# Performance work log

Measured on AMD Instinct MI355X. Metric: run time of the kernel, lower is better.

## Reference

```python
import jax, jax.numpy as jnp
import numpy as np

REG1 = 0.05
REG2 = 0.05

N, D, P = 262144, 256, 512


def setup_inputs() -> dict:
    key = jax.random.key(0)
    kz, kp = jax.random.split(key)
    z = jax.random.normal(kz, (N, D), dtype=jnp.float32)
    # nn.Parameter(torch.rand(P, D)) -> uniform [0, 1)
    prototype_vectors = jax.random.uniform(kp, (P, D), dtype=jnp.float32)
    return {"z": z, "prototype_vectors": prototype_vectors}


def _cdist(a, b):
    # Euclidean pairwise distances [Na, Nb] via the norm trick (matches torch.cdist p=2).
    a2 = jnp.sum(a * a, axis=-1, keepdims=True)          # [Na, 1]
    b2 = jnp.sum(b * b, axis=-1)[None, :]                # [1, Nb]
    sq = a2 + b2 - 2.0 * (a @ b.T)
    return jnp.sqrt(jnp.maximum(sq, 0.0))


def reference(z, prototype_vectors):
    p_dist = _cdist(z, prototype_vectors)                # [N, P]
    f_dist = _cdist(prototype_vectors, z)                # [P, N]
    return (REG1 * jnp.mean(jnp.min(p_dist, axis=1))
            + REG2 * jnp.mean(jnp.min(f_dist, axis=1)))
```

## Files before the change

### kernel.cpp

```cpp
#include <hip/hip_runtime.h>
#include <hip/hip_bf16.h>

#define N_ROWS 262144
#define DDIM   256
#define PROTO  512
#define BM     64
#define RTG    4096
#define NBLK   8192

typedef __bf16 bf16x8 __attribute__((ext_vector_type(8)));
typedef float  f32x4  __attribute__((ext_vector_type(4)));

__global__ void prep_proto(const float* __restrict__ Pm,
                           unsigned short* __restrict__ PBf,
                           float* __restrict__ P2) {
  int p = blockIdx.x;
  int k = threadIdx.x;
  float v = Pm[p * DDIM + k];
  int idx = (p >> 4) * 4096 + (k >> 5) * 512 + ((((k >> 3) & 3) * 16) + (p & 15)) * 8 + (k & 7);
  ((__bf16*)PBf)[idx] = (__bf16)v;
  float sq = v * v;
  #pragma unroll
  for (int m = 1; m < 64; m <<= 1) sq += __shfl_xor(sq, m);
  __shared__ float ws4[4];
  if ((k & 63) == 0) ws4[k >> 6] = sq;
  __syncthreads();
  if (k == 0) P2[p] = (ws4[0] + ws4[1]) + (ws4[2] + ws4[3]);
}

__global__ __launch_bounds__(256, 4)
void proto_main(const float* __restrict__ Z, const unsigned short* __restrict__ PBf,
                const float* __restrict__ P2, float* __restrict__ colpart,
                float* __restrict__ rowminpart) {
  __shared__ __align__(16) unsigned short A_lds[BM * 256];
  __shared__ float z2s[BM];
  __shared__ float rowred[BM * 4];

  const int t   = threadIdx.x;
  const int w   = t >> 6;
  const int l   = t & 63;
  const int l15 = l & 15;
  const int lg  = l >> 4;

  const int bid = blockIdx.x;
  const int g   = ((bid >> 4) << 3) | (bid & 7);
  const int cc  = (bid >> 3) & 1;
  const size_t row0 = (size_t)g * BM;

  const int srow = t >> 2;
  const int sc4  = t & 3;
  {
    const float4* Zv = (const float4*)Z + (row0 + srow) * (DDIM / 4);
    float4 za[16];
    #pragma unroll
    for (int m = 0; m < 8; ++m) {
      za[2 * m]     = Zv[(sc4 + m * 4) * 2];
      za[2 * m + 1] = Zv[(sc4 + m * 4) * 2 + 1];
    }
    float zacc = 0.f;
    #pragma unroll
    for (int m = 0; m < 8; ++m) {
      float4 a0 = za[2 * m], a1 = za[2 * m + 1];
      zacc += a0.x*a0.x + a0.y*a0.y + a0.z*a0.z + a0.w*a0.w
            + a1.x*a1.x + a1.y*a1.y + a1.z*a1.z + a1.w*a1.w;
      bf16x8 pk;
      pk[0] = (__bf16)a0.x; pk[1] = (__bf16)a0.y; pk[2] = (__bf16)a0.z; pk[3] = (__bf16)a0.w;
      pk[4] = (__bf16)a1.x; pk[5] = (__bf16)a1.y; pk[6] = (__bf16)a1.z; pk[7] = (__bf16)a1.w;
      int slot = (sc4 + m * 4) ^ (srow & 7);
      *(bf16x8*)&A_lds[srow * 256 + slot * 8] = pk;
    }
    zacc += __shfl_xor(zacc, 1);
    zacc += __shfl_xor(zacc, 2);
    if (sc4 == 0) z2s[srow] = zacc;
  }

  float p2r[4];
  #pragma unroll
  for (int j = 0; j < 4; ++j) p2r[j] = P2[cc * 256 + w * 64 + j * 16 + l15];

  __syncthreads();

  f32x4 acc[4][4];
  #pragma unroll
  for (int i = 0; i < 4; ++i)
    #pragma unroll
    for (int j = 0; j < 4; ++j)
      acc[i][j] = (f32x4){0.f, 0.f, 0.f, 0.f};

  const unsigned short* PBw = PBf + (size_t)(cc * 16 + w * 4) * 4096 + l * 8;
  bf16x8 bgn[4];
  #pragma unroll
  for (int j = 0; j < 4; ++j)
    bgn[j] = *(const bf16x8*)&PBw[(size_t)(j * 8) * 512];
  #pragma unroll
  for (int ks = 0; ks < 8; ++ks) {
    bf16x8 bgc[4];
    #pragma unroll
    for (int j = 0; j < 4; ++j) bgc[j] = bgn[j];
    if (ks < 7) {
      #pragma unroll
      for (int j = 0; j < 4; ++j)
        bgn[j] = *(const bf16x8*)&PBw[(size_t)(j * 8 + ks + 1) * 512];
    }
    __builtin_amdgcn_s_setprio(1);
    #pragma unroll
    for (int i = 0; i < 4; ++i) {
      bf16x8 af = *(const bf16x8*)&A_lds[(i * 16 + l15) * 256 + (((ks * 4 + lg) ^ (l15 & 7)) * 8)];
      #pragma unroll
      for (int j = 0; j < 4; ++j)
        acc[i][j] = __builtin_amdgcn_mfma_f32_16x16x32_bf16(af, bgc[j], acc[i][j], 0, 0, 0);
    }
    __builtin_amdgcn_s_setprio(0);
  }

  float cmin[4] = {3.4e38f, 3.4e38f, 3.4e38f, 3.4e38f};
  #pragma unroll
  for (int i = 0; i < 4; ++i) {
    #pragma unroll
    for (int r = 0; r < 4; ++r) {
      int arow = i * 16 + lg * 4 + r;
      float z2 = z2s[arow];
      float m = 3.4e38f;
      #pragma unroll
      for (int j = 0; j < 4; ++j) {
        float sq = fmaxf(z2 + p2r[j] - 2.0f * acc[i][j][r], 0.0f);
        m = fminf(m, sq);
        cmin[j] = fminf(cmin[j], sq);
      }
      m = fminf(m, __shfl_xor(m, 1));
      m = fminf(m, __shfl_xor(m, 2));
      m = fminf(m, __shfl_xor(m, 4));
      m = fminf(m, __shfl_xor(m, 8));
      if (l15 == 0) rowred[arow * 4 + w] = m;
    }
  }
  #pragma unroll
  for (int j = 0; j < 4; ++j) {
    float c = cmin[j];
    c = fminf(c, __shfl_xor(c, 16));
    c = fminf(c, __shfl_xor(c, 32));
    cmin[j] = c;
  }
  if (l < 16) {
    #pragma unroll
    for (int j = 0; j < 4; ++j)
      colpart[(size_t)g * PROTO + cc * 256 + w * 64 + j * 16 + l] = cmin[j];
  }
  __syncthreads();
  if (t < 64) {
    float m = fminf(fminf(rowred[t * 4], rowred[t * 4 + 1]),
                    fminf(rowred[t * 4 + 2], rowred[t * 4 + 3]));
    rowminpart[(size_t)cc * N_ROWS + row0 + t] = m;
  }
}

__global__ void col_reduce(const float* __restrict__ colpart, float* __restrict__ colfin) {
  int t    = threadIdx.x;
  int colb = blockIdx.x * 16;
  int cl   = t & 15;
  int gg   = t >> 4;
  float m = 3.4e38f;
  for (int g = gg; g < RTG; g += 32)
    m = fminf(m, colpart[(size_t)g * PROTO + colb + cl]);
  m = fminf(m, __shfl_xor(m, 16));
  m = fminf(m, __shfl_xor(m, 32));
  __shared__ float red[8][16];
  if ((t & 63) < 16) red[t >> 6][cl] = m;
  __syncthreads();
  if (t < 16) {
    float r = red[0][t];
    #pragma unroll
    for (int wv = 1; wv < 8; ++wv) r = fminf(r, red[wv][t]);
    colfin[colb + t] = sqrtf(r);
  }
}

__global__ void row_reduce(const float* __restrict__ rowminpart, float* __restrict__ rowsum) {
  int t = threadIdx.x;
  size_t grow = (size_t)blockIdx.x * 256 + t;
  float m = fminf(rowminpart[grow], rowminpart[N_ROWS + grow]);
  float s = sqrtf(m);
  #pragma unroll
  for (int mm = 1; mm < 64; mm <<= 1) s += __shfl_xor(s, mm);
  __shared__ float ws4[4];
  if ((t & 63) == 0) ws4[t >> 6] = s;
  __syncthreads();
  if (t == 0) rowsum[blockIdx.x] = (ws4[0] + ws4[1]) + (ws4[2] + ws4[3]);
}

__global__ void final_reduce(const float* __restrict__ colfin,
                             const float* __restrict__ rowsum,
                             float* __restrict__ out) {
  int t = threadIdx.x;
  float sc = colfin[t];
  float sr = rowsum[t] + rowsum[t + 512];
  #pragma unroll
  for (int mm = 1; mm < 64; mm <<= 1) { sc += __shfl_xor(sc, mm); sr += __shfl_xor(sr, mm); }
  __shared__ float wc[8], wr[8];
  if ((t & 63) == 0) { wc[t >> 6] = sc; wr[t >> 6] = sr; }
  __syncthreads();
  if (t == 0) {
    float tc = 0.f, tr = 0.f;
    #pragma unroll
    for (int i = 0; i < 8; ++i) { tc += wc[i]; tr += wr[i]; }
    out[0] = 0.05f * (tr / (float)N_ROWS) + 0.05f * (tc / (float)PROTO);
  }
}

extern "C" void kernel_launch(void* const* d_in, const int* in_sizes, int n_in,
                              void* d_out, int out_size, void* d_ws, size_t ws_size,
                              hipStream_t stream) {
  const float* z  = (const float*)d_in[0];
  const float* pv = (const float*)d_in[1];
  char* ws = (char*)d_ws;
  size_t off = 0;
  unsigned short* PBf = (unsigned short*)(ws + off); off += 262144;
  float* P2           = (float*)(ws + off);          off += 2048;
  float* colpart      = (float*)(ws + off);          off += (size_t)RTG * PROTO * 4;
  float* colfin       = (float*)(ws + off);          off += 2048;
  float* rowminpart   = (float*)(ws + off);          off += (size_t)2 * N_ROWS * 4;
  float* rowsum       = (float*)(ws + off);          off += 4096;

  prep_proto<<<PROTO, DDIM, 0, stream>>>(pv, PBf, P2);
  proto_main<<<NBLK, 256, 0, stream>>>(z, PBf, P2, colpart, rowminpart);
  col_reduce<<<32, 512, 0, stream>>>(colpart, colfin);
  row_reduce<<<N_ROWS / 256, 256, 0, stream>>>(rowminpart, rowsum);
  final_reduce<<<1, PROTO, 0, stream>>>(colfin, rowsum, (float*)d_out);
}
```

Before: 140.6 us.

## Double row tile per block to 128 rows with eight waves

```diff
diff --git a/kernel.cpp b/kernel.cpp
--- a/kernel.cpp
+++ b/kernel.cpp
@@ -4,9 +4,9 @@
 #define N_ROWS 262144
 #define DDIM   256
 #define PROTO  512
-#define BM     64
-#define RTG    4096
-#define NBLK   8192
+#define BM2    128
+#define RTG    2048
+#define NBLK   4096
 
 typedef __bf16 bf16x8 __attribute__((ext_vector_type(8)));
 typedef float  f32x4  __attribute__((ext_vector_type(4)));
@@ -28,24 +28,27 @@
   if (k == 0) P2[p] = (ws4[0] + ws4[1]) + (ws4[2] + ws4[3]);
 }
 
-__global__ __launch_bounds__(256, 4)
+__global__ __launch_bounds__(512, 4)
 void proto_main(const float* __restrict__ Z, const unsigned short* __restrict__ PBf,
                 const float* __restrict__ P2, float* __restrict__ colpart,
                 float* __restrict__ rowminpart) {
-  __shared__ __align__(16) unsigned short A_lds[BM * 256];
-  __shared__ float z2s[BM];
-  __shared__ float rowred[BM * 4];
+  __shared__ __align__(16) unsigned short A_lds[BM2 * 256];
+  __shared__ float z2s[BM2];
+  __shared__ float rowred[BM2 * 4];
+  __shared__ float colred[2 * 256];
 
   const int t   = threadIdx.x;
   const int w   = t >> 6;
   const int l   = t & 63;
   const int l15 = l & 15;
   const int lg  = l >> 4;
+  const int wr  = w >> 2;
+  const int wc  = w & 3;
 
   const int bid = blockIdx.x;
   const int g   = ((bid >> 4) << 3) | (bid & 7);
   const int cc  = (bid >> 3) & 1;
-  const size_t row0 = (size_t)g * BM;
+  const size_t row0 = (size_t)g * BM2;
 
   const int srow = t >> 2;
   const int sc4  = t & 3;
@@ -76,7 +79,7 @@
 
   float p2r[4];
   #pragma unroll
-  for (int j = 0; j < 4; ++j) p2r[j] = P2[cc * 256 + w * 64 + j * 16 + l15];
+  for (int j = 0; j < 4; ++j) p2r[j] = P2[cc * 256 + wc * 64 + j * 16 + l15];
 
   __syncthreads();
 
@@ -87,7 +90,7 @@
     for (int j = 0; j < 4; ++j)
       acc[i][j] = (f32x4){0.f, 0.f, 0.f, 0.f};
 
-  const unsigned short* PBw = PBf + (size_t)(cc * 16 + w * 4) * 4096 + l * 8;
+  const unsigned short* PBw = PBf + (size_t)(cc * 16 + wc * 4) * 4096 + l * 8;
   bf16x8 bgn[4];
   #pragma unroll
   for (int j = 0; j < 4; ++j)
@@ -105,7 +108,8 @@
     __builtin_amdgcn_s_setprio(1);
     #pragma unroll
     for (int i = 0; i < 4; ++i) {
-      bf16x8 af = *(const bf16x8*)&A_lds[(i * 16 + l15) * 256 + (((ks * 4 + lg) ^ (l15 & 7)) * 8)];
+      bf16x8 af = *(const bf16x8*)&A_lds[(wr * 64 + i * 16 + l15) * 256 +
+                                         (((ks * 4 + lg) ^ (l15 & 7)) * 8)];
       #pragma unroll
       for (int j = 0; j < 4; ++j)
         acc[i][j] = __builtin_amdgcn_mfma_f32_16x16x32_bf16(af, bgc[j], acc[i][j], 0, 0, 0);
@@ -118,12 +122,12 @@
   for (int i = 0; i < 4; ++i) {
     #pragma unroll
     for (int r = 0; r < 4; ++r) {
-      int arow = i * 16 + lg * 4 + r;
+      int arow = wr * 64 + i * 16 + lg * 4 + r;
       float z2 = z2s[arow];
       float m = 3.4e38f;
       #pragma unroll
       for (int j = 0; j < 4; ++j) {
-        float sq = fmaxf(z2 + p2r[j] - 2.0f * acc[i][j][r], 0.0f);
+        float sq = fmaxf(fmaf(acc[i][j][r], -2.0f, z2 + p2r[j]), 0.0f);
         m = fminf(m, sq);
         cmin[j] = fminf(cmin[j], sq);
       }
@@ -131,7 +135,7 @@
       m = fminf(m, __shfl_xor(m, 2));
       m = fminf(m, __shfl_xor(m, 4));
       m = fminf(m, __shfl_xor(m, 8));
-      if (l15 == 0) rowred[arow * 4 + w] = m;
+      if (l15 == 0) rowred[arow * 4 + wc] = m;
     }
   }
   #pragma unroll
@@ -144,13 +148,18 @@
   if (l < 16) {
     #pragma unroll
     for (int j = 0; j < 4; ++j)
-      colpart[(size_t)g * PROTO + cc * 256 + w * 64 + j * 16 + l] = cmin[j];
-  }
-  __syncthreads();
-  if (t < 64) {
-    float m = fminf(fminf(rowred[t * 4], rowred[t * 4 + 1]),
-                    fminf(rowred[t * 4 + 2], rowred[t * 4 + 3]));
-    rowminpart[(size_t)cc * N_ROWS + row0 + t] = m;
+      colred[wr * 256 + wc * 64 + j * 16 + l] = cmin[j];
+  }
+  __syncthreads();
+
+  if (t < 256) {
+    colpart[(size_t)g * PROTO + cc * 256 + t] = fminf(colred[t], colred[256 + t]);
+  }
+  if (t >= 256 && t < 256 + BM2) {
+    int rr = t - 256;
+    float m = fminf(fminf(rowred[rr * 4], rowred[rr * 4 + 1]),
+                    fminf(rowred[rr * 4 + 2], rowred[rr * 4 + 3]));
+    rowminpart[(size_t)cc * N_ROWS + row0 + rr] = m;
   }
 }
 
@@ -222,7 +231,7 @@
   float* rowsum       = (float*)(ws + off);          off += 4096;
 
   prep_proto<<<PROTO, DDIM, 0, stream>>>(pv, PBf, P2);
-  proto_main<<<NBLK, 256, 0, stream>>>(z, PBf, P2, colpart, rowminpart);
+  proto_main<<<NBLK, 512, 0, stream>>>(z, PBf, P2, colpart, rowminpart);
   col_reduce<<<32, 512, 0, stream>>>(colpart, colfin);
   row_reduce<<<N_ROWS / 256, 256, 0, stream>>>(rowminpart, rowsum);
   final_reduce<<<1, PROTO, 0, stream>>>(colfin, rowsum, (float*)d_out);
```

Measured after the change: 142.7 us. Within noise of the previous version (+1.5%).
